# Kernel tuning notes

Hardware: AMD Instinct MI355X
Metric: run time of the kernel (lower is better)

## Reference

```python
import jax, jax.numpy as jnp
import numpy as np

N_NODES = 100_000
N_EDGES = 600_000
D = 128  # in_channels


def setup_inputs() -> dict:
    key = jax.random.key(0)
    k1, k2, k3, k4, k5 = jax.random.split(key, 5)
    node_embs_src = jax.random.normal(k1, (N_NODES, D), dtype=jnp.float32)
    node_embs_dst = jax.random.normal(k2, (N_NODES, D), dtype=jnp.float32)
    edge_index = jax.random.randint(k3, (2, N_EDGES), 0, N_NODES, dtype=jnp.int64)
    # MLP params: Linear(2D -> D), Linear(D -> 1); scaled like default torch init
    W1 = jax.random.normal(k4, (2 * D, D), dtype=jnp.float32) / np.sqrt(2 * D)
    b1 = jnp.zeros((D,), dtype=jnp.float32)
    W2 = jax.random.normal(k5, (D, 1), dtype=jnp.float32) / np.sqrt(D)
    b2 = jnp.zeros((1,), dtype=jnp.float32)
    return {
        "node_embs_src": node_embs_src,
        "node_embs_dst": node_embs_dst,
        "edge_index": edge_index,
        "W1": W1,
        "b1": b1,
        "W2": W2,
        "b2": b2,
    }


def reference(node_embs_src, node_embs_dst, edge_index, W1, b1, W2, b2):
    # Gather per-edge source / destination embeddings: [E, D] each
    src = node_embs_src[edge_index[0]]
    dst = node_embs_dst[edge_index[1]]
    # concat([src, dst]) @ W1 == src @ W1[:D] + dst @ W1[D:]  (avoids materializing [E, 2D])
    h = jnp.dot(src, W1[:D]) + jnp.dot(dst, W1[D:]) + b1  # [E, D]
    h = jax.nn.relu(h)
    logits = jnp.dot(h, W2) + b2  # [E, 1]
    return jax.nn.sigmoid(logits)
```

## Files before the change

### kernel.cpp

```cpp
#include <hip/hip_runtime.h>
#include <stdint.h>

typedef __attribute__((ext_vector_type(8))) short short8;
typedef __attribute__((ext_vector_type(4))) float f32x4;

__device__ __forceinline__ unsigned short f2bf(float f) {
  union { float f; uint32_t u; } v; v.f = f;
  uint32_t u = v.u;
  uint32_t r = (u + 0x7FFFu + ((u >> 16) & 1u)) >> 16;
  return (unsigned short)r;
}
__device__ __forceinline__ float bf2f(unsigned short h) {
  union { uint32_t u; float f; } v; v.u = ((uint32_t)h) << 16; return v.f;
}

#define NBM 64
__global__ __launch_bounds__(256, 4)
void node_phase_kernel(const float* __restrict__ src_emb,
                       const float* __restrict__ dst_emb,
                       const float* __restrict__ W1,
                       const float* __restrict__ b1,
                       unsigned short* __restrict__ UV,
                       int Nn, int ntiles) {
  __shared__ __align__(16) char Als[NBM * 256];

  const int tbl = blockIdx.y;
  const float* emb = tbl ? dst_emb : src_emb;
  const float* Wt  = W1 + (size_t)tbl * 128 * 128;
  unsigned short* outp = UV + (size_t)tbl * Nn * 128;

  const int tid  = threadIdx.x;
  const int lane = tid & 63;
  const int w    = tid >> 6;
  const int l15  = lane & 15;
  const int lk8  = (lane >> 4) * 8;

  short8 bfrag[4][2];
#pragma unroll
  for (int s = 0; s < 4; ++s) {
#pragma unroll
    for (int nf = 0; nf < 2; ++nf) {
      const int col = w * 32 + 2 * l15 + nf;
      short8 t;
#pragma unroll
      for (int j = 0; j < 8; ++j) {
        const int k = s * 32 + lk8 + j;
        t[j] = (short)f2bf(Wt[k * 128 + col]);
      }
      bfrag[s][nf] = t;
    }
  }
  const int colb = w * 32 + 2 * l15;
  const float bias0 = tbl ? 0.f : b1[colb];
  const float bias1 = tbl ? 0.f : b1[colb + 1];

  const int q = tid & 15, r0 = tid >> 4;
  const int swz = (l15 & 7) << 4;
  const int gx = gridDim.x;

  float4 p0[4], p1[4];
#pragma unroll
  for (int i = 0; i < 4; ++i) {
    const int node = blockIdx.x * NBM + i * 16 + r0;
    if (node < Nn) {
      const float* base = emb + (size_t)node * 128 + q * 8;
      p0[i] = *(const float4*)base;
      p1[i] = *(const float4*)(base + 4);
    }
  }

  for (int t = blockIdx.x; t < ntiles; t += gx) {
    const int t0 = t * NBM;

#pragma unroll
    for (int i = 0; i < 4; ++i) {
      const int row = i * 16 + r0;
      short8 hv;
      hv[0] = (short)f2bf(p0[i].x); hv[1] = (short)f2bf(p0[i].y);
      hv[2] = (short)f2bf(p0[i].z); hv[3] = (short)f2bf(p0[i].w);
      hv[4] = (short)f2bf(p1[i].x); hv[5] = (short)f2bf(p1[i].y);
      hv[6] = (short)f2bf(p1[i].z); hv[7] = (short)f2bf(p1[i].w);
      const int byteoff = row * 256 + ((q * 16) ^ ((row & 7) << 4));
      *(short8*)(Als + byteoff) = hv;
    }
    __syncthreads();

    const int tn = t + gx;
    if (tn < ntiles) {
#pragma unroll
      for (int i = 0; i < 4; ++i) {
        const int node = tn * NBM + i * 16 + r0;
        if (node < Nn) {
          const float* base = emb + (size_t)node * 128 + q * 8;
          p0[i] = *(const float4*)base;
          p1[i] = *(const float4*)(base + 4);
        }
      }
    }

#pragma unroll
    for (int m = 0; m < 4; ++m) {
      f32x4 acc0 = {0.f, 0.f, 0.f, 0.f};
      f32x4 acc1 = {0.f, 0.f, 0.f, 0.f};
      const int rowb = (m * 16 + l15) * 256;
      const int kb0  = lk8 * 2;
#pragma unroll
      for (int s = 0; s < 4; ++s) {
        const int off = rowb + ((s * 64 + kb0) ^ swz);
        const short8 a = *(const short8*)(Als + off);
        acc0 = __builtin_amdgcn_mfma_f32_16x16x32_bf16(a, bfrag[s][0], acc0, 0, 0, 0);
        acc1 = __builtin_amdgcn_mfma_f32_16x16x32_bf16(a, bfrag[s][1], acc1, 0, 0, 0);
      }
#pragma unroll
      for (int reg = 0; reg < 4; ++reg) {
        const int orow = t0 + m * 16 + ((lane >> 4) * 4) + reg;
        if (orow < Nn) {
          const uint32_t pk = (uint32_t)f2bf(acc0[reg] + bias0) |
                              ((uint32_t)f2bf(acc1[reg] + bias1) << 16);
          *(uint32_t*)&outp[(size_t)orow * 128 + colb] = pk;
        }
      }
    }
    __syncthreads();
  }
}

#define PREFETCH_PAIR(eL, su0, sv0, su1, sv1)                                  \
  {                                                                            \
    const int _e0 = (eL), _e1 = (eL) + stride;                                 \
    const int _i0 = _e0 < E ? _e0 : 0;                                         \
    const int _i1 = _e1 < E ? _e1 : 0;                                         \
    const uint32_t _s0 = (uint32_t)eidx[_i0], _d0 = (uint32_t)eidx[E + _i0];   \
    const uint32_t _s1 = (uint32_t)eidx[_i1], _d1 = (uint32_t)eidx[E + _i1];   \
    su0 = *(const short8*)(U + (size_t)_s0 * 128 + l15 * 8);                   \
    sv0 = *(const short8*)(V + (size_t)_d0 * 128 + l15 * 8);                   \
    su1 = *(const short8*)(U + (size_t)_s1 * 128 + l15 * 8);                   \
    sv1 = *(const short8*)(V + (size_t)_d1 * 128 + l15 * 8);                   \
  }

#define COMPUTE_PAIR(eL, su0, sv0, su1, sv1)                                   \
  {                                                                            \
    float _a0 = 0.f, _a1 = 0.f;                                                \
    _Pragma("unroll") for (int _c = 0; _c < 8; ++_c) {                         \
      float _g0 = bf2f((unsigned short)su0[_c]) + bf2f((unsigned short)sv0[_c]); \
      float _g1 = bf2f((unsigned short)su1[_c]) + bf2f((unsigned short)sv1[_c]); \
      _g0 = _g0 > 0.f ? _g0 : 0.f;                                             \
      _g1 = _g1 > 0.f ? _g1 : 0.f;                                             \
      _a0 = fmaf(_g0, w2s[_c], _a0);                                           \
      _a1 = fmaf(_g1, w2s[_c], _a1);                                           \
    }                                                                          \
    _Pragma("unroll") for (int _off = 1; _off < 16; _off <<= 1) {              \
      _a0 += __shfl_xor(_a0, _off, 64);                                        \
      _a1 += __shfl_xor(_a1, _off, 64);                                        \
    }                                                                          \
    if (l15 == 0) {                                                            \
      const int _e0 = (eL), _e1 = (eL) + stride;                               \
      if (_e0 < E) out[_e0] = 1.f / (1.f + __expf(-(_a0 + b2s)));              \
      if (_e1 < E) out[_e1] = 1.f / (1.f + __expf(-(_a1 + b2s)));              \
    }                                                                          \
  }

__global__ __launch_bounds__(256, 8)
void edge_phase_kernel(const unsigned short* __restrict__ UV,
                       const int* __restrict__ eidx,
                       const float* __restrict__ W2,
                       const float* __restrict__ b2,
                       float* __restrict__ out,
                       int E, int Nn) {
  const int tid = threadIdx.x;
  const int l15 = tid & 15;
  const int sg  = tid >> 4;

  float w2s[8];
#pragma unroll
  for (int j = 0; j < 8; ++j) w2s[j] = W2[l15 * 8 + j];
  const float b2s = b2[0];
  const unsigned short* U = UV;
  const unsigned short* V = UV + (size_t)Nn * 128;

  const int stride = gridDim.x * 16;
  const int step   = stride * 2;

  int e_lo = blockIdx.x * 16 + sg;

  short8 uA0, vA0, uA1, vA1;
  short8 uB0, vB0, uB1, vB1;
  PREFETCH_PAIR(e_lo, uA0, vA0, uA1, vA1);

  for (;;) {
    {
      const int e_nxt = e_lo + step;
      PREFETCH_PAIR(e_nxt, uB0, vB0, uB1, vB1);
      COMPUTE_PAIR(e_lo, uA0, vA0, uA1, vA1);
      e_lo = e_nxt;
      if (e_lo >= E) break;
    }
    {
      const int e_nxt = e_lo + step;
      PREFETCH_PAIR(e_nxt, uA0, vA0, uA1, vA1);
      COMPUTE_PAIR(e_lo, uB0, vB0, uB1, vB1);
      e_lo = e_nxt;
      if (e_lo >= E) break;
    }
  }
}

#define BM 64
__global__ __launch_bounds__(256, 4)
void edge_decoder_fused(const float* __restrict__ src_emb,
                        const float* __restrict__ dst_emb,
                        const int* __restrict__ eidx,
                        const float* __restrict__ W1,
                        const float* __restrict__ b1,
                        const float* __restrict__ W2,
                        const float* __restrict__ b2,
                        float* __restrict__ out,
                        int E, int ntiles) {
  __shared__ __align__(16) char Als[BM * 512];
  __shared__ float rowpart[4][BM];

  const int tid  = threadIdx.x;
  const int lane = tid & 63;
  const int w    = tid >> 6;
  const int l15  = lane & 15;
  const int lk8  = (lane >> 4) * 8;

  short8 bfrag[8][2];
#pragma unroll
  for (int s = 0; s < 8; ++s) {
#pragma unroll
    for (int nf = 0; nf < 2; ++nf) {
      const int col = w * 32 + nf * 16 + l15;
      short8 t;
#pragma unroll
      for (int j = 0; j < 8; ++j) {
        const int k = s * 32 + lk8 + j;
        t[j] = (short)f2bf(W1[k * 128 + col]);
      }
      bfrag[s][nf] = t;
    }
  }
  float b1v[2], w2v[2];
#pragma unroll
  for (int nf = 0; nf < 2; ++nf) {
    const int col = w * 32 + nf * 16 + l15;
    b1v[nf] = b1[col];
    w2v[nf] = W2[col];
  }
  const float b2s = b2[0];

  const int q  = tid & 31;
  const int r0 = tid >> 5;
  const int qq = q & 15;
  const bool is_src = (q < 16);
  const int swz = (l15 & 7) << 4;

  for (int t = blockIdx.x; t < ntiles; t += gridDim.x) {
    const int t0 = t * BM;
#pragma unroll
    for (int i = 0; i < 8; ++i) {
      const int row = i * 8 + r0;
      const int e = t0 + row;
      if (e < E) {
        const int node = is_src ? eidx[e] : eidx[E + e];
        const float* base = (is_src ? src_emb : dst_emb) + (size_t)node * 128 + qq * 8;
        const float4 f0 = *(const float4*)base;
        const float4 f1 = *(const float4*)(base + 4);
        short8 hv;
        hv[0] = (short)f2bf(f0.x); hv[1] = (short)f2bf(f0.y);
        hv[2] = (short)f2bf(f0.z); hv[3] = (short)f2bf(f0.w);
        hv[4] = (short)f2bf(f1.x); hv[5] = (short)f2bf(f1.y);
        hv[6] = (short)f2bf(f1.z); hv[7] = (short)f2bf(f1.w);
        const int byteoff = row * 512 + ((q * 16) ^ ((row & 7) << 4));
        *(short8*)(Als + byteoff) = hv;
      }
    }
    __syncthreads();

    for (int m = 0; m < 4; ++m) {
      f32x4 acc0 = {0.f, 0.f, 0.f, 0.f};
      f32x4 acc1 = {0.f, 0.f, 0.f, 0.f};
      const int rowb = (m * 16 + l15) * 512;
      const int kb0  = lk8 * 2;
#pragma unroll
      for (int s = 0; s < 8; ++s) {
        const int off = rowb + ((s * 64 + kb0) ^ swz);
        const short8 a = *(const short8*)(Als + off);
        acc0 = __builtin_amdgcn_mfma_f32_16x16x32_bf16(a, bfrag[s][0], acc0, 0, 0, 0);
        acc1 = __builtin_amdgcn_mfma_f32_16x16x32_bf16(a, bfrag[s][1], acc1, 0, 0, 0);
      }
      float pr[4];
#pragma unroll
      for (int reg = 0; reg < 4; ++reg) {
        float h0 = acc0[reg] + b1v[0]; h0 = h0 > 0.f ? h0 : 0.f;
        float h1 = acc1[reg] + b1v[1]; h1 = h1 > 0.f ? h1 : 0.f;
        pr[reg] = h0 * w2v[0] + h1 * w2v[1];
      }
#pragma unroll
      for (int off = 1; off < 16; off <<= 1) {
#pragma unroll
        for (int reg = 0; reg < 4; ++reg)
          pr[reg] += __shfl_xor(pr[reg], off, 64);
      }
      if (l15 == 0) {
        const int rbase = m * 16 + (lane >> 4) * 4;
#pragma unroll
        for (int reg = 0; reg < 4; ++reg)
          rowpart[w][rbase + reg] = pr[reg];
      }
    }
    __syncthreads();

    if (tid < BM) {
      const int e = t0 + tid;
      if (e < E) {
        const float sum = rowpart[0][tid] + rowpart[1][tid] +
                          rowpart[2][tid] + rowpart[3][tid] + b2s;
        out[e] = 1.f / (1.f + __expf(-sum));
      }
    }
    __syncthreads();
  }
}

extern "C" void kernel_launch(void* const* d_in, const int* in_sizes, int n_in,
                              void* d_out, int out_size, void* d_ws, size_t ws_size,
                              hipStream_t stream) {
  const float* src = (const float*)d_in[0];
  const float* dst = (const float*)d_in[1];
  const int*   eix = (const int*)d_in[2];
  const float* W1  = (const float*)d_in[3];
  const float* b1  = (const float*)d_in[4];
  const float* W2  = (const float*)d_in[5];
  const float* b2  = (const float*)d_in[6];
  float* out = (float*)d_out;

  const int E  = in_sizes[2] / 2;
  const int Nn = in_sizes[0] / 128;
  const size_t uv_bytes = (size_t)Nn * 128 * 2 * sizeof(unsigned short);

  if (ws_size >= uv_bytes) {
    unsigned short* UV = (unsigned short*)d_ws;
    const int ntiles_n = (Nn + NBM - 1) / NBM;
    const int gx = ntiles_n < 512 ? ntiles_n : 512;
    node_phase_kernel<<<dim3(gx, 2), 256, 0, stream>>>(src, dst, W1, b1, UV, Nn, ntiles_n);
    const int nblk = ((E + 15) / 16 < 2048) ? (E + 15) / 16 : 2048;
    edge_phase_kernel<<<nblk, 256, 0, stream>>>(UV, eix, W2, b2, out, E, Nn);
  } else {
    const int ntiles = (E + BM - 1) / BM;
    const int grid = ntiles < 2048 ? ntiles : 2048;
    edge_decoder_fused<<<grid, 256, 0, stream>>>(src, dst, eix, W1, b1, W2, b2,
                                                 out, E, ntiles);
  }
}
```

Baseline: 76.99 us.

## Load edge indices coalesced per block and broadcast via shuffles in edge phase

The edge kernel now assigns each block a contiguous chunk of 256 edges. Each thread loads one src/dst index pair with a coalesced load, and 16-lane groups broadcast the indices with __shfl to fetch U/V rows for 16 consecutive edges in turn. Indices for the next chunk are prefetched, and the row loads are software-pipelined with double buffering. This replaces redundant per-lane scattered index loads and uses width-16 shuffles for the reduction, at the cost of a sequential 16-edge loop per group and less in-flight memory parallelism per thread.

```diff
diff --git a/kernel.cpp b/kernel.cpp
--- a/kernel.cpp
+++ b/kernel.cpp
@@ -125,38 +125,29 @@
   }
 }
 
-#define PREFETCH_PAIR(eL, su0, sv0, su1, sv1)                                  \
+#define LOAD_ROWS(sreg, dreg, KK, su, sv)                                      \
   {                                                                            \
-    const int _e0 = (eL), _e1 = (eL) + stride;                                 \
-    const int _i0 = _e0 < E ? _e0 : 0;                                         \
-    const int _i1 = _e1 < E ? _e1 : 0;                                         \
-    const uint32_t _s0 = (uint32_t)eidx[_i0], _d0 = (uint32_t)eidx[E + _i0];   \
-    const uint32_t _s1 = (uint32_t)eidx[_i1], _d1 = (uint32_t)eidx[E + _i1];   \
-    su0 = *(const short8*)(U + (size_t)_s0 * 128 + l15 * 8);                   \
-    sv0 = *(const short8*)(V + (size_t)_d0 * 128 + l15 * 8);                   \
-    su1 = *(const short8*)(U + (size_t)_s1 * 128 + l15 * 8);                   \
-    sv1 = *(const short8*)(V + (size_t)_d1 * 128 + l15 * 8);                   \
-  }
-
-#define COMPUTE_PAIR(eL, su0, sv0, su1, sv1)                                   \
+    const uint32_t _s = (uint32_t)__shfl(sreg, (KK), 16);                      \
+    const uint32_t _d = (uint32_t)__shfl(dreg, (KK), 16);                      \
+    su = *(const short8*)(U + (size_t)_s * 128 + l15 * 8);                     \
+    sv = *(const short8*)(V + (size_t)_d * 128 + l15 * 8);                     \
+  }
+
+#define COMPUTE_E(KK, su, sv)                                                  \
   {                                                                            \
-    float _a0 = 0.f, _a1 = 0.f;                                                \
+    float _acc = 0.f;                                                          \
     _Pragma("unroll") for (int _c = 0; _c < 8; ++_c) {                         \
-      float _g0 = bf2f((unsigned short)su0[_c]) + bf2f((unsigned short)sv0[_c]); \
-      float _g1 = bf2f((unsigned short)su1[_c]) + bf2f((unsigned short)sv1[_c]); \
-      _g0 = _g0 > 0.f ? _g0 : 0.f;                                             \
-      _g1 = _g1 > 0.f ? _g1 : 0.f;                                             \
-      _a0 = fmaf(_g0, w2s[_c], _a0);                                           \
-      _a1 = fmaf(_g1, w2s[_c], _a1);                                           \
+      float _g = bf2f((unsigned short)su[_c]) + bf2f((unsigned short)sv[_c]);  \
+      _g = _g > 0.f ? _g : 0.f;                                                \
+      _acc = fmaf(_g, w2s[_c], _acc);                                          \
     }                                                                          \
-    _Pragma("unroll") for (int _off = 1; _off < 16; _off <<= 1) {              \
-      _a0 += __shfl_xor(_a0, _off, 64);                                        \
-      _a1 += __shfl_xor(_a1, _off, 64);                                        \
-    }                                                                          \
+    _acc += __shfl_xor(_acc, 1, 16);                                           \
+    _acc += __shfl_xor(_acc, 2, 16);                                           \
+    _acc += __shfl_xor(_acc, 4, 16);                                           \
+    _acc += __shfl_xor(_acc, 8, 16);                                           \
     if (l15 == 0) {                                                            \
-      const int _e0 = (eL), _e1 = (eL) + stride;                               \
-      if (_e0 < E) out[_e0] = 1.f / (1.f + __expf(-(_a0 + b2s)));              \
-      if (_e1 < E) out[_e1] = 1.f / (1.f + __expf(-(_a1 + b2s)));              \
+      const int _e = ebase_sg + (KK);                                          \
+      if (_e < E) out[_e] = 1.f / (1.f + __expf(-(_acc + b2s)));               \
     }                                                                          \
   }
 
@@ -169,7 +160,6 @@
                        int E, int Nn) {
   const int tid = threadIdx.x;
   const int l15 = tid & 15;
-  const int sg  = tid >> 4;
 
   float w2s[8];
 #pragma unroll
@@ -178,30 +168,54 @@
   const unsigned short* U = UV;
   const unsigned short* V = UV + (size_t)Nn * 128;
 
-  const int stride = gridDim.x * 16;
-  const int step   = stride * 2;
-
-  int e_lo = blockIdx.x * 16 + sg;
-
-  short8 uA0, vA0, uA1, vA1;
-  short8 uB0, vB0, uB1, vB1;
-  PREFETCH_PAIR(e_lo, uA0, vA0, uA1, vA1);
+  const int gstep = gridDim.x * 256;
+  int base = blockIdx.x * 256;
+  if (base >= E) return;
+
+  int eb0 = base + tid; eb0 = eb0 < E ? eb0 : E - 1;
+  int sidxA = eidx[eb0];
+  int didxA = eidx[E + eb0];
+  int sidxB, didxB;
+
+  short8 uA, vA, uB, vB;
+  {
+    int ebase_sg_dummy; (void)ebase_sg_dummy;
+    const uint32_t _s = (uint32_t)__shfl(sidxA, 0, 16);
+    const uint32_t _d = (uint32_t)__shfl(didxA, 0, 16);
+    uA = *(const short8*)(U + (size_t)_s * 128 + l15 * 8);
+    vA = *(const short8*)(V + (size_t)_d * 128 + l15 * 8);
+  }
 
   for (;;) {
+    const int ebase_sg = base + (tid & 0xF0);
+    const int nbase = base + gstep;
+
     {
-      const int e_nxt = e_lo + step;
-      PREFETCH_PAIR(e_nxt, uB0, vB0, uB1, vB1);
-      COMPUTE_PAIR(e_lo, uA0, vA0, uA1, vA1);
-      e_lo = e_nxt;
-      if (e_lo >= E) break;
-    }
-    {
-      const int e_nxt = e_lo + step;
-      PREFETCH_PAIR(e_nxt, uA0, vA0, uA1, vA1);
-      COMPUTE_PAIR(e_lo, uB0, vB0, uB1, vB1);
-      e_lo = e_nxt;
-      if (e_lo >= E) break;
-    }
+      int ebn = nbase + tid; ebn = ebn < E ? ebn : E - 1;
+      sidxB = eidx[ebn];
+      didxB = eidx[E + ebn];
+    }
+
+#pragma unroll
+    for (int k2 = 0; k2 < 8; ++k2) {
+      const int k = 2 * k2;
+      LOAD_ROWS(sidxA, didxA, k + 1, uB, vB);
+      COMPUTE_E(k, uA, vA);
+      if (k2 < 7) {
+        LOAD_ROWS(sidxA, didxA, k + 2, uA, vA);
+      } else if (nbase < E) {
+        const uint32_t _s = (uint32_t)__shfl(sidxB, 0, 16);
+        const uint32_t _d = (uint32_t)__shfl(didxB, 0, 16);
+        uA = *(const short8*)(U + (size_t)_s * 128 + l15 * 8);
+        vA = *(const short8*)(V + (size_t)_d * 128 + l15 * 8);
+      }
+      COMPUTE_E(k + 1, uB, vB);
+    }
+
+    if (nbase >= E) break;
+    base = nbase;
+    sidxA = sidxB;
+    didxA = didxB;
   }
 }
 
@@ -344,7 +358,8 @@
     const int ntiles_n = (Nn + NBM - 1) / NBM;
     const int gx = ntiles_n < 512 ? ntiles_n : 512;
     node_phase_kernel<<<dim3(gx, 2), 256, 0, stream>>>(src, dst, W1, b1, UV, Nn, ntiles_n);
-    const int nblk = ((E + 15) / 16 < 2048) ? (E + 15) / 16 : 2048;
+    const int nchunks = (E + 255) / 256;
+    const int nblk = nchunks < 2048 ? nchunks : 2048;
     edge_phase_kernel<<<nblk, 256, 0, stream>>>(UV, eix, W2, b2, out, E, Nn);
   } else {
     const int ntiles = (E + BM - 1) / BM;
```

New measurement: 77.84 us. No clear change (+1.1%).
